# Optimization experiments

Hardware: AMD Instinct MI355X
Metric: run time of the kernel (lower is better)

## Reference

```python
import jax, jax.numpy as jnp
import numpy as np

K = 2048          # codes per class
NC = 8            # num_classes
CD = 256          # conv_dims
SP = 4            # latent spatial (28 -> 14 -> 7 -> 4)
D = CD * SP * SP  # 4096 codebook vector dim
N = 512           # RoIs


def _conv(x, W, b, stride, pad):
    y = jax.lax.conv_general_dilated(x, W, (stride, stride), [(pad, pad), (pad, pad)],
                                     dimension_numbers=('NCHW', 'OIHW', 'NCHW'))
    return y + b[None, :, None, None]


def _upsample2_ac(x):
    # bilinear upsample x2 with align_corners=True (torch nn.Upsample semantics)
    n, ch, H, W = x.shape
    Ho, Wo = 2 * H, 2 * W
    ys = jnp.arange(Ho) * (H - 1) / (Ho - 1)
    xs = jnp.arange(Wo) * (W - 1) / (Wo - 1)
    y0 = jnp.floor(ys).astype(jnp.int32); y1 = jnp.minimum(y0 + 1, H - 1)
    x0 = jnp.floor(xs).astype(jnp.int32); x1 = jnp.minimum(x0 + 1, W - 1)
    wy = (ys - y0).astype(x.dtype); wx = (xs - x0).astype(x.dtype)
    r = x[:, :, y0, :] * (1 - wy)[None, None, :, None] + x[:, :, y1, :] * wy[None, None, :, None]
    return r[:, :, :, x0] * (1 - wx)[None, None, None, :] + r[:, :, :, x1] * wx[None, None, None, :]


def setup_inputs() -> dict:
    key = jax.random.key(0)
    ks = jax.random.split(key, 20)
    s = 0.02
    inp = {
        'x': jax.random.normal(ks[0], (N, 1, 28, 28), jnp.float32),
        'We0': jax.random.normal(ks[1], (CD, 1, 3, 3), jnp.float32) * s,
        'be0': jnp.zeros((CD,), jnp.float32),
        'We1': jax.random.normal(ks[2], (CD, CD, 3, 3), jnp.float32) * s,
        'be1': jnp.zeros((CD,), jnp.float32),
        'We2': jax.random.normal(ks[3], (CD, CD, 3, 3), jnp.float32) * s,
        'be2': jnp.zeros((CD,), jnp.float32),
        'E': jax.random.normal(ks[4], (K * NC, D), jnp.float32) * s,
        'Wd0': jax.random.normal(ks[5], (CD, CD, 3, 3), jnp.float32) * s,
        'bd0': jnp.zeros((CD,), jnp.float32),
        'Wd1': jax.random.normal(ks[6], (CD, CD, 3, 3), jnp.float32) * s,
        'bd1': jnp.zeros((CD,), jnp.float32),
        'Wd2': jax.random.normal(ks[7], (CD, CD, 3, 3), jnp.float32) * s,
        'bd2': jnp.zeros((CD,), jnp.float32),
        'Wo': jax.random.normal(ks[8], (1, CD, 3, 3), jnp.float32) * s,
        'bo': jnp.zeros((1,), jnp.float32),
        'c': jax.random.randint(ks[9], (N,), 0, NC, jnp.int32),
    }
    return inp


def reference(x, We0, be0, We1, be1, We2, be2, E, Wd0, bd0, Wd1, bd1, Wd2, bd2, Wo, bo, c):
    # ---- encoder: 3 stride-2 convs, relu on all but the last ----
    h = jax.nn.relu(_conv(x, We0, be0, 2, 1))   # [N,CD,14,14]
    h = jax.nn.relu(_conv(h, We1, be1, 2, 1))   # [N,CD,7,7]
    h = _conv(h, We2, be2, 2, 1)                # [N,CD,4,4]
    z_e = h.reshape(N, D)                       # flattened latent, == z_e_x [N,D,1,1]

    # ---- class-conditional VQ ----
    # torch code loops over unique classes and concatenates -> output is in
    # stable-sorted-by-class order; replicate via stable argsort permutation.
    perm = jnp.argsort(c)  # stable
    # distances to the FULL table, then mask codes outside the sample's class slice
    d2 = (jnp.sum(z_e * z_e, axis=1, keepdims=True)         # [N,1]
          - 2.0 * z_e @ E.T                                  # [N,K*NC]
          + jnp.sum(E * E, axis=1)[None, :])
    code_cls = jnp.arange(K * NC, dtype=c.dtype) // K        # class of each code row
    d2 = jnp.where(code_cls[None, :] == c[:, None], d2, jnp.inf)
    idx = jnp.argmin(d2, axis=1)                             # global code index (includes key*K offset)

    q_det = jax.lax.stop_gradient(E)[idx]                    # vq_st uses detached codebook
    z_q_st = z_e + jax.lax.stop_gradient(q_det - z_e)        # straight-through
    z_q_bar = E[idx]                                         # gradient flows to codebook

    z_q_st_p = z_q_st[perm]
    z_q_bar_p = z_q_bar[perm]

    # ---- decoder: (upsample2 bilinear ac + conv + relu) x3, pad=0 on layer k==num_conv-2 ----
    xd = z_q_st_p.reshape(N, CD, SP, SP)
    xd = jax.nn.relu(_conv(_upsample2_ac(xd), Wd0, bd0, 1, 1))  # 4->8
    xd = jax.nn.relu(_conv(_upsample2_ac(xd), Wd1, bd1, 1, 0))  # 8->16->14
    xd = jax.nn.relu(_conv(_upsample2_ac(xd), Wd2, bd2, 1, 1))  # 14->28
    x_tilde = jax.nn.sigmoid(_conv(xd, Wo, bo, 1, 1))           # [N,1,28,28]

    return (x_tilde, z_e.reshape(N, D, 1, 1), z_q_bar_p.reshape(N, D, 1, 1))
```

## Files before the change

### kernel.cpp

```cpp
#include <hip/hip_runtime.h>
#include <hip/hip_bf16.h>
#include <cstdint>
#include <cstddef>

#define CDIV(a,b) (((a)+(b)-1)/(b))

typedef __attribute__((ext_vector_type(8))) short vbf8;
typedef __attribute__((ext_vector_type(4))) float vf4;

__device__ inline unsigned short f2bf(float f) {
  unsigned u = __float_as_uint(f);
  unsigned r = (u + 0x7fffu + ((u >> 16) & 1u)) >> 16;
  return (unsigned short)r;
}
__device__ inline float bf2f(unsigned short h) { return __uint_as_float(((unsigned)h) << 16); }

__global__ __launch_bounds__(256) void conv_e0_cl_kernel(
    const float* __restrict__ x, const float* __restrict__ W,
    const float* __restrict__ b, unsigned short* __restrict__ hi,
    unsigned short* __restrict__ lo)
{
  __shared__ float s_img[784];
  const int n = blockIdx.x;
  const int co = threadIdx.x;
  for (int i = threadIdx.x; i < 784; i += 256) s_img[i] = x[(size_t)n*784 + i];
  float w[9];
#pragma unroll
  for (int t = 0; t < 9; ++t) w[t] = W[co*9 + t];
  const float bb = b[co];
  __syncthreads();
  for (int p = 0; p < 196; ++p) {
    int y = p / 14, xo = p % 14;
    float a = bb;
#pragma unroll
    for (int t = 0; t < 9; ++t) {
      int yi = 2*y + t/3 - 1, xi = 2*xo + t%3 - 1;
      if (yi >= 0 && yi < 28 && xi >= 0 && xi < 28) a = fmaf(w[t], s_img[yi*28 + xi], a);
    }
    a = fmaxf(a, 0.f);
    unsigned short h = f2bf(a);
    size_t oidx = ((size_t)n*196 + p)*256 + co;
    hi[oidx] = h;
    lo[oidx] = f2bf(a - bf2f(h));
  }
}

__global__ __launch_bounds__(256) void wprep2_kernel(
    const float* __restrict__ W, unsigned short* __restrict__ Whi,
    unsigned short* __restrict__ Wlo)
{
  int idx = blockIdx.x*256 + threadIdx.x;
  if (idx >= 589824) return;
  int j   = idx & 7;
  int co  = (idx >> 3) & 255;
  int cig = (idx >> 11) & 31;
  int t   = idx >> 16;
  int ci  = cig*8 + j;
  float w = W[((size_t)co*256 + ci)*9 + t];
  unsigned short h = f2bf(w);
  Whi[idx] = h;
  Wlo[idx] = f2bf(w - bf2f(h));
}

template<int STRIDE, int HO, int WO, int X0, int WOP, int ROWS, int HI, int WI,
         int PAD, int ACT, int SPLIT, int OUTMODE>
__global__ __launch_bounds__(256, 2) void convmfma_kernel(
    const unsigned short* __restrict__ inT, const unsigned short* __restrict__ inTlo,
    const vbf8* __restrict__ Wt, const vbf8* __restrict__ Wtlo,
    const float* __restrict__ bias,
    unsigned short* __restrict__ outT, unsigned short* __restrict__ outTlo,
    float* __restrict__ outF)
{
  constexpr int NFM = ROWS*WOP/16;
  constexpr int RIN = (ROWS-1)*STRIDE + 3;
  constexpr int WS  = (WOP-1)*STRIDE + 3;
  constexpr int NG  = SPLIT ? 12 : 4;
  __shared__ vbf8 sA[RIN*WS*8];

  const int n  = blockIdx.x;
  const int y0 = blockIdx.y * ROWS;
  const int tid = threadIdx.x;
  const int lane = tid & 63;
  const int wv = tid >> 6;
  const int l15 = lane & 15;
  const int lq  = lane >> 4;
  const int cobase = wv * 64;

  int abase[NFM];
#pragma unroll
  for (int mf = 0; mf < NFM; ++mf) {
    int pos = mf*16 + l15;
    abase[mf] = (pos / WOP) * STRIDE * WS + (pos % WOP) * STRIDE;
  }

  vf4 acc[NFM][4];
#pragma unroll
  for (int mf = 0; mf < NFM; ++mf)
#pragma unroll
    for (int nf = 0; nf < 4; ++nf) acc[mf][nf] = (vf4){0.f, 0.f, 0.f, 0.f};

#pragma unroll 1
  for (int g = 0; g < NG; ++g) {
    const int cc = g & 3;
    const unsigned short* src = (SPLIT && g >= 8) ? inTlo : inT;
    const vbf8* wsrc = (SPLIT && g >= 4 && g < 8) ? Wtlo : Wt;
    for (int idx = tid; idx < RIN*WS*8; idx += 256) {
      int lin = idx >> 3, cig = idx & 7;
      int r = lin / WS, x = lin % WS;
      int yi = y0*STRIDE + r - PAD, xi = X0*STRIDE + x - PAD;
      vbf8 v = {0,0,0,0,0,0,0,0};
      if (yi >= 0 && yi < HI && xi >= 0 && xi < WI)
        v = *(const vbf8*)(src + ((((size_t)n*HI + yi)*WI + xi)*256 + cc*64 + cig*8));
      sA[(lin*8 + cig) ^ (lin & 7)] = v;
    }
    __syncthreads();
#pragma unroll
    for (int t = 0; t < 9; ++t) {
      const int dy = t/3, dx = t%3;
#pragma unroll
      for (int kk = 0; kk < 2; ++kk) {
        vbf8 bfr[4];
        const int cig_g = cc*8 + kk*4 + lq;
#pragma unroll
        for (int nf = 0; nf < 4; ++nf)
          bfr[nf] = wsrc[((size_t)t*32 + cig_g)*256 + cobase + nf*16 + l15];
        vbf8 af[NFM];
        const int cigl = kk*4 + lq;
#pragma unroll
        for (int mf = 0; mf < NFM; ++mf) {
          int lin = abase[mf] + dy*WS + dx;
          af[mf] = sA[(lin*8 + cigl) ^ (lin & 7)];
        }
#pragma unroll
        for (int mf = 0; mf < NFM; ++mf)
#pragma unroll
          for (int nf = 0; nf < 4; ++nf)
            acc[mf][nf] = __builtin_amdgcn_mfma_f32_16x16x32_bf16(af[mf], bfr[nf], acc[mf][nf], 0, 0, 0);
      }
    }
    __syncthreads();
  }

  float bb[4];
#pragma unroll
  for (int nf = 0; nf < 4; ++nf) bb[nf] = bias[cobase + nf*16 + l15];
#pragma unroll
  for (int mf = 0; mf < NFM; ++mf) {
#pragma unroll
    for (int q = 0; q < 4; ++q) {
      int pos = mf*16 + lq*4 + q;
      int y = y0 + pos/WOP, x = X0 + pos % WOP;
      if (X0 + WOP > WO && x >= WO) continue;
      if (HO % ROWS != 0 && y >= HO) continue;
#pragma unroll
      for (int nf = 0; nf < 4; ++nf) {
        float v = acc[mf][nf][q] + bb[nf];
        if (ACT) v = fmaxf(v, 0.f);
        const int co = cobase + nf*16 + l15;
        if (OUTMODE == 2) {
          outF[((size_t)n*256 + co)*(HO*WO) + y*WO + x] = v;
        } else {
          size_t oidx = (((size_t)n*HO + y)*WO + x)*256 + co;
          unsigned short h = f2bf(v);
          outT[oidx] = h;
          if (OUTMODE == 1) outTlo[oidx] = f2bf(v - bf2f(h));
        }
      }
    }
  }
}

template<int H, int W>
__global__ __launch_bounds__(256) void upsample_cl_kernel(
    const unsigned short* __restrict__ in, unsigned short* __restrict__ out, int nimg)
{
  constexpr int Ho = 2*H, Wo = 2*W;
  int idx = blockIdx.x*256 + threadIdx.x;
  int total = nimg * Ho * Wo * 32;
  if (idx >= total) return;
  int cig = idx & 31; int rest = idx >> 5;
  int xo = rest % Wo; rest /= Wo;
  int yo = rest % Ho; int n = rest / Ho;
  float ys = (float)(yo*(H-1)) / (float)(Ho-1);
  float xs = (float)(xo*(W-1)) / (float)(Wo-1);
  int ya = (int)ys; int yb = (ya+1 < H) ? ya+1 : H-1;
  int xa = (int)xs; int xb = (xa+1 < W) ? xa+1 : W-1;
  float wy = ys - (float)ya, wx = xs - (float)xa;
  const unsigned short* base = in + (size_t)n*H*W*256 + cig*8;
  vbf8 vaa = *(const vbf8*)(base + ((size_t)ya*W + xa)*256);
  vbf8 vab = *(const vbf8*)(base + ((size_t)ya*W + xb)*256);
  vbf8 vba = *(const vbf8*)(base + ((size_t)yb*W + xa)*256);
  vbf8 vbb = *(const vbf8*)(base + ((size_t)yb*W + xb)*256);
  vbf8 o;
#pragma unroll
  for (int j = 0; j < 8; ++j) {
    float r0 = bf2f((unsigned short)vaa[j])*(1.f-wy) + bf2f((unsigned short)vba[j])*wy;
    float r1 = bf2f((unsigned short)vab[j])*(1.f-wy) + bf2f((unsigned short)vbb[j])*wy;
    o[j] = (short)f2bf(r0*(1.f-wx) + r1*wx);
  }
  *(vbf8*)(out + (((size_t)n*Ho + yo)*Wo + xo)*256 + cig*8) = o;
}

__global__ __launch_bounds__(256) void conv_out_t_kernel(
    const unsigned short* __restrict__ a2t, const float* __restrict__ Wo,
    const float* __restrict__ bo, float* __restrict__ out)
{
  const int n = blockIdx.x;
  const int y0 = blockIdx.y * 14;
  const int tid = threadIdx.x;
  __shared__ vbf8 s_in[16*30*8];
  __shared__ float s_w[9*64];
  float acc[2] = {0.f, 0.f};
  for (int cc = 0; cc < 4; ++cc) {
    for (int idx = tid; idx < 16*30*8; idx += 256) {
      int lin = idx >> 3, cig = idx & 7;
      int r = lin / 30, xx = lin % 30;
      int yi = y0 + r - 1, xi = xx - 1;
      vbf8 v = {0,0,0,0,0,0,0,0};
      if (yi >= 0 && yi < 28 && xi >= 0 && xi < 28)
        v = *(const vbf8*)(a2t + (((size_t)n*28 + yi)*28 + xi)*256 + cc*64 + cig*8);
      s_in[(lin*8 + cig) ^ (lin & 7)] = v;
    }
    for (int idx = tid; idx < 576; idx += 256) {
      int t = idx / 64, cil = idx % 64;
      s_w[t*64 + cil] = Wo[((size_t)cc*64 + cil)*9 + t];
    }
    __syncthreads();
#pragma unroll
    for (int q = 0; q < 2; ++q) {
      int p = tid + q*256;
      if (p < 392) {
        int y = p / 28, x = p % 28;
        float a = acc[q];
#pragma unroll
        for (int t = 0; t < 9; ++t) {
          int lin = (y + t/3)*30 + (x + t%3);
#pragma unroll
          for (int cig = 0; cig < 8; ++cig) {
            vbf8 v = s_in[(lin*8 + cig) ^ (lin & 7)];
#pragma unroll
            for (int j = 0; j < 8; ++j)
              a = fmaf(bf2f((unsigned short)v[j]), s_w[t*64 + cig*8 + j], a);
          }
        }
        acc[q] = a;
      }
    }
    __syncthreads();
  }
  const float bb = bo[0];
  for (int q = 0; q < 2; ++q) {
    int p = tid + q*256;
    if (p < 392) {
      int y = y0 + p/28, x = p%28;
      out[(size_t)n*784 + y*28 + x] = 1.f/(1.f + expf(-(acc[q] + bb)));
    }
  }
}

__global__ __launch_bounds__(256) void enorm_kernel(
    const float* __restrict__ E, float* __restrict__ norms)
{
  const int k = blockIdx.x;
  const float4* row = (const float4*)(E + (size_t)k*4096);
  float s = 0.f;
  for (int i = threadIdx.x; i < 1024; i += 256) {
    float4 v = row[i];
    s += v.x*v.x + v.y*v.y + v.z*v.z + v.w*v.w;
  }
  __shared__ float red[256];
  red[threadIdx.x] = s; __syncthreads();
  for (int off = 128; off > 0; off >>= 1) {
    if (threadIdx.x < off) red[threadIdx.x] += red[threadIdx.x + off];
    __syncthreads();
  }
  if (threadIdx.x == 0) norms[k] = red[0];
}

__global__ __launch_bounds__(256) void etrans_kernel(
    const float* __restrict__ E, unsigned short* __restrict__ Et)
{
  const int cb = blockIdx.x;
  const int kb = blockIdx.y;
  const int t = threadIdx.x;
  const int cl = t >> 2;
  const int seg = t & 3;
  const int code = cb*64 + cl;
  const int k0 = kb*64 + seg*16;
  const float4* src = (const float4*)(E + (size_t)code*4096 + k0);
  float4 v0 = src[0], v1 = src[1], v2 = src[2], v3 = src[3];
  vbf8 a, b;
  a[0]=(short)f2bf(v0.x); a[1]=(short)f2bf(v0.y); a[2]=(short)f2bf(v0.z); a[3]=(short)f2bf(v0.w);
  a[4]=(short)f2bf(v1.x); a[5]=(short)f2bf(v1.y); a[6]=(short)f2bf(v1.z); a[7]=(short)f2bf(v1.w);
  b[0]=(short)f2bf(v2.x); b[1]=(short)f2bf(v2.y); b[2]=(short)f2bf(v2.z); b[3]=(short)f2bf(v2.w);
  b[4]=(short)f2bf(v3.x); b[5]=(short)f2bf(v3.y); b[6]=(short)f2bf(v3.z); b[7]=(short)f2bf(v3.w);
  vbf8* dst = (vbf8*)Et;
  dst[(size_t)(k0 >> 3)*16384 + code]     = a;
  dst[((size_t)(k0 >> 3) + 1)*16384 + code] = b;
}

__global__ __launch_bounds__(512) void perm_kernel(
    const int* __restrict__ c, int* __restrict__ perm, int* __restrict__ off)
{
  __shared__ int sc[512];
  __shared__ int cnt[8];
  __shared__ int base[9];
  const int i = threadIdx.x;
  sc[i] = c[i];
  if (i < 8) cnt[i] = 0;
  __syncthreads();
  atomicAdd(&cnt[sc[i]], 1);
  __syncthreads();
  if (i == 0) { int a = 0; for (int j = 0; j < 8; ++j) { base[j] = a; a += cnt[j]; } base[8] = a; }
  __syncthreads();
  const int ci = sc[i];
  int rank = 0;
  for (int j = 0; j < i; ++j) rank += (sc[j] == ci) ? 1 : 0;
  perm[base[ci] + rank] = i;
  if (i < 9) off[i] = base[i];
}

__global__ __launch_bounds__(256) void vq_coarse_kernel(
    const float* __restrict__ zE, const vbf8* __restrict__ Etv,
    const float* __restrict__ norms, const int* __restrict__ perm,
    const int* __restrict__ offs, float* __restrict__ dco)
{
  const int cls = blockIdx.x;
  const int mb  = blockIdx.y;
  const int kb  = blockIdx.z;
  const int s0 = offs[cls];
  const int total = offs[cls+1] - s0;
  int nrows = total - mb*64;
  if (nrows <= 0) return;
  if (nrows > 64) nrows = 64;

  __shared__ vbf8 sA[64*8];
  __shared__ int srow_s[64];
  const int tid = threadIdx.x;
  if (tid < 64) srow_s[tid] = (tid < nrows) ? perm[s0 + mb*64 + tid] : -1;
  __syncthreads();

  const int lane = tid & 63;
  const int wv = tid >> 6;
  const int l15 = lane & 15;
  const int lq  = lane >> 4;

  const int myrow = tid >> 2;
  const int seg = tid & 3;
  const int srow_mine = srow_s[myrow];
  const float* zbase = (srow_mine >= 0) ? (zE + (size_t)srow_mine*4096 + seg*16) : nullptr;

  const int cbase = cls*2048 + kb*256 + wv*64;

  vf4 acc[4][4];
#pragma unroll
  for (int mf = 0; mf < 4; ++mf)
#pragma unroll
    for (int nf = 0; nf < 4; ++nf) acc[mf][nf] = (vf4){0.f, 0.f, 0.f, 0.f};

#pragma unroll 1
  for (int k0 = 0; k0 < 4096; k0 += 64) {
    {
      float4 v0, v1, v2, v3;
      if (zbase) {
        const float4* p = (const float4*)(zbase + k0);
        v0 = p[0]; v1 = p[1]; v2 = p[2]; v3 = p[3];
      } else {
        v0 = v1 = v2 = v3 = (float4){0.f, 0.f, 0.f, 0.f};
      }
      vbf8 a, b;
      a[0]=(short)f2bf(v0.x); a[1]=(short)f2bf(v0.y); a[2]=(short)f2bf(v0.z); a[3]=(short)f2bf(v0.w);
      a[4]=(short)f2bf(v1.x); a[5]=(short)f2bf(v1.y); a[6]=(short)f2bf(v1.z); a[7]=(short)f2bf(v1.w);
      b[0]=(short)f2bf(v2.x); b[1]=(short)f2bf(v2.y); b[2]=(short)f2bf(v2.z); b[3]=(short)f2bf(v2.w);
      b[4]=(short)f2bf(v3.x); b[5]=(short)f2bf(v3.y); b[6]=(short)f2bf(v3.z); b[7]=(short)f2bf(v3.w);
      int c0 = seg*2;
      sA[myrow*8 + (c0 ^ (myrow & 7))]       = a;
      sA[myrow*8 + ((c0 + 1) ^ (myrow & 7))] = b;
    }
    __syncthreads();
#pragma unroll
    for (int kb32 = 0; kb32 < 2; ++kb32) {
      vbf8 af[4], bf[4];
#pragma unroll
      for (int mf = 0; mf < 4; ++mf) {
        int row = mf*16 + l15;
        af[mf] = sA[row*8 + ((kb32*4 + lq) ^ (row & 7))];
      }
      const size_t kg = (size_t)((k0 >> 3) + kb32*4 + lq);
#pragma unroll
      for (int nf = 0; nf < 4; ++nf)
        bf[nf] = Etv[kg*16384 + cbase + nf*16 + l15];
#pragma unroll
      for (int mf = 0; mf < 4; ++mf)
#pragma unroll
        for (int nf = 0; nf < 4; ++nf)
          acc[mf][nf] = __builtin_amdgcn_mfma_f32_16x16x32_bf16(af[mf], bf[nf], acc[mf][nf], 0, 0, 0);
    }
    __syncthreads();
  }

  float nrm[4];
#pragma unroll
  for (int nf = 0; nf < 4; ++nf) nrm[nf] = norms[cbase + nf*16 + l15];
#pragma unroll
  for (int mf = 0; mf < 4; ++mf) {
#pragma unroll
    for (int q = 0; q < 4; ++q) {
      int slot = mf*16 + lq*4 + q;
      if (slot < nrows) {
        int s = srow_s[slot];
        float* drow = dco + (size_t)s*2048 + (kb*256 + wv*64);
#pragma unroll
        for (int nf = 0; nf < 4; ++nf)
          drow[nf*16 + l15] = nrm[nf] - 2.f*acc[mf][nf][q];
      }
    }
  }
}

__global__ __launch_bounds__(256) void vq_select_kernel(
    const float* __restrict__ dco, const int* __restrict__ c,
    const float* __restrict__ zE, const float* __restrict__ E,
    int* __restrict__ codes)
{
  const int s = blockIdx.x;
  const int cls = c[s];
  const int tid = threadIdx.x;
  const float* drow = dco + (size_t)s*2048;

  float mn = 3.4e38f, mx = -3.4e38f;
  for (int j = tid; j < 2048; j += 256) {
    float d = drow[j];
    mn = fminf(mn, d); mx = fmaxf(mx, d);
  }
  __shared__ float smn[256], smx[256];
  smn[tid] = mn; smx[tid] = mx;
  __syncthreads();
  for (int o = 128; o > 0; o >>= 1) {
    if (tid < o) { smn[tid] = fminf(smn[tid], smn[tid+o]); smx[tid] = fmaxf(smx[tid], smx[tid+o]); }
    __syncthreads();
  }
  const float dmin = smn[0], dmax = smx[0];
  const float margin = 0.06f*(dmax - dmin) + 1e-6f*fabsf(dmin) + 1e-20f;

  __shared__ int cand[64];
  __shared__ int cnt_s;
  if (tid == 0) cnt_s = 0;
  __syncthreads();
  for (int j = tid; j < 2048; j += 256) {
    if (drow[j] <= dmin + margin) {
      int p = atomicAdd(&cnt_s, 1);
      if (p < 64) cand[p] = j;
    }
  }
  __syncthreads();
  const int cnt = (cnt_s < 64) ? cnt_s : 64;

  __shared__ double red[256];
  __shared__ double bestd_s;
  __shared__ int bestc_s;
  if (tid == 0) { bestd_s = 1.0e300; bestc_s = 0x7fffffff; }
  __syncthreads();
  const float* zrow = zE + (size_t)s*4096;
  for (int t = 0; t < cnt; ++t) {
    const int gcode = cls*2048 + cand[t];
    const float* erow = E + (size_t)gcode*4096;
    double p = 0.0;
    for (int e2 = tid; e2 < 4096; e2 += 256) {
      double ev = (double)erow[e2];
      double zv = (double)zrow[e2];
      p += ev*ev - 2.0*zv*ev;
    }
    red[tid] = p;
    __syncthreads();
    for (int o = 128; o > 0; o >>= 1) {
      if (tid < o) red[tid] += red[tid+o];
      __syncthreads();
    }
    if (tid == 0) {
      double d = red[0];
      if (d < bestd_s || (d == bestd_s && gcode < bestc_s)) { bestd_s = d; bestc_s = gcode; }
    }
    __syncthreads();
  }
  if (tid == 0) codes[s] = bestc_s;
}

__global__ __launch_bounds__(256) void gather_t_kernel(
    const int* __restrict__ codes, const int* __restrict__ perm,
    const float* __restrict__ E, float* __restrict__ zq, unsigned short* __restrict__ zqt)
{
  const int i = blockIdx.x;
  const int s = perm[i];
  const int code = codes[s];
  const float4* src = (const float4*)(E + (size_t)code*4096);
  float4* dst = (float4*)(zq + (size_t)i*4096);
  for (int t = threadIdx.x; t < 1024; t += 256) {
    float4 v = src[t];
    dst[t] = v;
    int e0 = t*4;
    int ci = e0 >> 4, sp = e0 & 15;
    unsigned short* zp = zqt + ((size_t)i*16 + sp)*256 + ci;
    zp[0]   = f2bf(v.x);
    zp[256] = f2bf(v.y);
    zp[512] = f2bf(v.z);
    zp[768] = f2bf(v.w);
  }
}

extern "C" void kernel_launch(void* const* d_in, const int* in_sizes, int n_in,
                              void* d_out, int out_size, void* d_ws, size_t ws_size,
                              hipStream_t stream) {
  const float* x   = (const float*)d_in[0];
  const float* We0 = (const float*)d_in[1];
  const float* be0 = (const float*)d_in[2];
  const float* We1 = (const float*)d_in[3];
  const float* be1 = (const float*)d_in[4];
  const float* We2 = (const float*)d_in[5];
  const float* be2 = (const float*)d_in[6];
  const float* E   = (const float*)d_in[7];
  const float* Wd0 = (const float*)d_in[8];
  const float* bd0 = (const float*)d_in[9];
  const float* Wd1 = (const float*)d_in[10];
  const float* bd1 = (const float*)d_in[11];
  const float* Wd2 = (const float*)d_in[12];
  const float* bd2 = (const float*)d_in[13];
  const float* Wo  = (const float*)d_in[14];
  const float* bo  = (const float*)d_in[15];
  const int*   c   = (const int*)d_in[16];

  float* out = (float*)d_out;
  float* z_e = out + (size_t)512*784;
  float* zq  = z_e + (size_t)512*4096;

  char* ws = (char*)d_ws;
  size_t off = 0;
  float* norms = (float*)(ws + off); off += 65536;
  int* codes = (int*)(ws + off); off += 2048;
  int* perm = (int*)(ws + off); off += 2048;
  int* offs = (int*)(ws + off); off += 256;
  float* dco = (float*)(ws + off); off += (size_t)512*2048*4;
  unsigned short* zqt = (unsigned short*)(ws + off); off += (size_t)512*16*256*2;
  unsigned short* Et = (unsigned short*)(ws + off); off += (size_t)512*16384*8*2;
  unsigned short* Wt0  = (unsigned short*)(ws + off); off += 1179648;
  unsigned short* Wt0l = (unsigned short*)(ws + off); off += 1179648;
  unsigned short* Wt1  = (unsigned short*)(ws + off); off += 1179648;
  unsigned short* Wt1l = (unsigned short*)(ws + off); off += 1179648;
  unsigned short* Wt2  = (unsigned short*)(ws + off); off += 1179648;
  unsigned short* Wt2l = (unsigned short*)(ws + off); off += 1179648;
  unsigned short* We1h = (unsigned short*)(ws + off); off += 1179648;
  unsigned short* We1l = (unsigned short*)(ws + off); off += 1179648;
  unsigned short* We2h = (unsigned short*)(ws + off); off += 1179648;
  unsigned short* We2l = (unsigned short*)(ws + off); off += 1179648;
  char* big = ws + off;
  size_t avail = (ws_size > off) ? ws_size - off : 0;

  int NB = 512;
  while (NB > 1 && (size_t)NB * 1350656ull > avail) NB >>= 1;
  const int nch = 512 / NB;

  size_t o = 0;
  unsigned short* h0h = (unsigned short*)(big + o); o += (size_t)NB*100352;
  unsigned short* h0l = (unsigned short*)(big + o); o += (size_t)NB*100352;
  unsigned short* h1h = (unsigned short*)(big + o); o += (size_t)NB*25088;
  unsigned short* h1l = (unsigned short*)(big + o); o += (size_t)NB*25088;
  unsigned short* u0t = (unsigned short*)(big + o); o += (size_t)NB*32768;
  unsigned short* a0t = (unsigned short*)(big + o); o += (size_t)NB*32768;
  unsigned short* u1t = (unsigned short*)(big + o); o += (size_t)NB*131072;
  unsigned short* a1t = (unsigned short*)(big + o); o += (size_t)NB*100352;
  unsigned short* u2t = (unsigned short*)(big + o); o += (size_t)NB*401408;
  unsigned short* a2t = (unsigned short*)(big + o); o += (size_t)NB*401408;

  wprep2_kernel<<<CDIV(589824,256), 256, 0, stream>>>(Wd0, Wt0, Wt0l);
  wprep2_kernel<<<CDIV(589824,256), 256, 0, stream>>>(Wd1, Wt1, Wt1l);
  wprep2_kernel<<<CDIV(589824,256), 256, 0, stream>>>(Wd2, Wt2, Wt2l);
  wprep2_kernel<<<CDIV(589824,256), 256, 0, stream>>>(We1, We1h, We1l);
  wprep2_kernel<<<CDIV(589824,256), 256, 0, stream>>>(We2, We2h, We2l);
  enorm_kernel<<<16384, 256, 0, stream>>>(E, norms);
  etrans_kernel<<<dim3(256,64), 256, 0, stream>>>(E, Et);

  for (int ch = 0; ch < nch; ++ch) {
    conv_e0_cl_kernel<<<NB, 256, 0, stream>>>(x + (size_t)ch*NB*784, We0, be0, h0h, h0l);
    convmfma_kernel<2,7,7,0,8,2, 14,14,1,1,1,1><<<dim3(NB,4), 256, 0, stream>>>(
        h0h, h0l, (const vbf8*)We1h, (const vbf8*)We1l, be1, h1h, h1l, nullptr);
    convmfma_kernel<2,4,4,0,4,4, 7,7,1,0,1,2><<<dim3(NB,1), 256, 0, stream>>>(
        h1h, h1l, (const vbf8*)We2h, (const vbf8*)We2l, be2, nullptr, nullptr,
        z_e + (size_t)ch*NB*4096);
  }
  perm_kernel<<<1, 512, 0, stream>>>(c, perm, offs);
  vq_coarse_kernel<<<dim3(8,8,8), 256, 0, stream>>>(
      z_e, (const vbf8*)Et, norms, perm, offs, dco);
  vq_select_kernel<<<512, 256, 0, stream>>>(dco, c, z_e, E, codes);
  gather_t_kernel<<<512, 256, 0, stream>>>(codes, perm, E, zq, zqt);

  for (int ch = 0; ch < nch; ++ch) {
    const unsigned short* zt = zqt + (size_t)ch*NB*16*256;
    upsample_cl_kernel<4,4><<<CDIV(NB*2048,256), 256, 0, stream>>>(zt, u0t, NB);
    convmfma_kernel<1,8,8,0,8,8, 8,8,1,1,0,0><<<dim3(NB,1), 256, 0, stream>>>(
        u0t, nullptr, (const vbf8*)Wt0, nullptr, bd0, a0t, nullptr, nullptr);
    upsample_cl_kernel<8,8><<<CDIV(NB*8192,256), 256, 0, stream>>>(a0t, u1t, NB);
    convmfma_kernel<1,14,14,0,16,4, 16,16,0,1,0,0><<<dim3(NB,4), 256, 0, stream>>>(
        u1t, nullptr, (const vbf8*)Wt1, nullptr, bd1, a1t, nullptr, nullptr);
    upsample_cl_kernel<14,14><<<CDIV(NB*25088,256), 256, 0, stream>>>(a1t, u2t, NB);
    convmfma_kernel<1,28,28,0,16,4, 28,28,1,1,0,0><<<dim3(NB,7), 256, 0, stream>>>(
        u2t, nullptr, (const vbf8*)Wt2, nullptr, bd2, a2t, nullptr, nullptr);
    convmfma_kernel<1,28,28,16,12,4, 28,28,1,1,0,0><<<dim3(NB,7), 256, 0, stream>>>(
        u2t, nullptr, (const vbf8*)Wt2, nullptr, bd2, a2t, nullptr, nullptr);
    conv_out_t_kernel<<<dim3(NB,2), 256, 0, stream>>>(a2t, Wo, bo, out + (size_t)ch*NB*784);
  }
}
```

Baseline: 1.969 ms.

## Double-buffer conv input tiles in LDS and retile encoder/decoder conv launches

```diff
diff --git a/kernel.cpp b/kernel.cpp
--- a/kernel.cpp
+++ b/kernel.cpp
@@ -62,8 +62,39 @@
   Wlo[idx] = f2bf(w - bf2f(h));
 }
 
+template<int NFM, int WS>
+__device__ __forceinline__ void mfma_block(
+    const vbf8* __restrict__ sbuf, const vbf8* __restrict__ wsrc, int cc,
+    const int (&abase)[NFM], vf4 (&acc)[NFM][4], int cobase, int l15, int lq)
+{
+#pragma unroll
+  for (int t = 0; t < 9; ++t) {
+    const int dy = t/3, dx = t%3;
+#pragma unroll
+    for (int kk = 0; kk < 2; ++kk) {
+      vbf8 bfr[4];
+      const int cig_g = cc*8 + kk*4 + lq;
+#pragma unroll
+      for (int nf = 0; nf < 4; ++nf)
+        bfr[nf] = wsrc[((size_t)t*32 + cig_g)*256 + cobase + nf*16 + l15];
+      vbf8 af[NFM];
+      const int cigl = kk*4 + lq;
+#pragma unroll
+      for (int mf = 0; mf < NFM; ++mf) {
+        int lin = abase[mf] + dy*WS + dx;
+        af[mf] = sbuf[(lin*8 + cigl) ^ (lin & 7)];
+      }
+#pragma unroll
+      for (int mf = 0; mf < NFM; ++mf)
+#pragma unroll
+        for (int nf = 0; nf < 4; ++nf)
+          acc[mf][nf] = __builtin_amdgcn_mfma_f32_16x16x32_bf16(af[mf], bfr[nf], acc[mf][nf], 0, 0, 0);
+    }
+  }
+}
+
 template<int STRIDE, int HO, int WO, int X0, int WOP, int ROWS, int HI, int WI,
-         int PAD, int ACT, int SPLIT, int OUTMODE>
+         int PAD, int ACT, int SPLIT, int OUTMODE, int DBUF>
 __global__ __launch_bounds__(256, 2) void convmfma_kernel(
     const unsigned short* __restrict__ inT, const unsigned short* __restrict__ inTlo,
     const vbf8* __restrict__ Wt, const vbf8* __restrict__ Wtlo,
@@ -75,7 +106,9 @@
   constexpr int RIN = (ROWS-1)*STRIDE + 3;
   constexpr int WS  = (WOP-1)*STRIDE + 3;
   constexpr int NG  = SPLIT ? 12 : 4;
-  __shared__ vbf8 sA[RIN*WS*8];
+  constexpr int NELEM = RIN*WS*8;
+  constexpr int CEIL = (NELEM + 255) / 256;
+  __shared__ vbf8 sA[DBUF ? 2 : 1][NELEM];
 
   const int n  = blockIdx.x;
   const int y0 = blockIdx.y * ROWS;
@@ -99,46 +132,73 @@
 #pragma unroll
     for (int nf = 0; nf < 4; ++nf) acc[mf][nf] = (vf4){0.f, 0.f, 0.f, 0.f};
 
+  if constexpr (DBUF) {
+    int goff[CEIL];
+#pragma unroll
+    for (int q = 0; q < CEIL; ++q) {
+      int idx = tid + q*256;
+      int lin = idx >> 3, cig = idx & 7;
+      int rr = lin / WS, xx = lin % WS;
+      int yi = y0*STRIDE + rr - PAD, xi = X0*STRIDE + xx - PAD;
+      bool ok = (idx < NELEM) && yi >= 0 && yi < HI && xi >= 0 && xi < WI;
+      goff[q] = ok ? (int)((((size_t)n*HI + yi)*WI + xi)*256 + cig*8) : -1;
+    }
+    vbf8 r[CEIL];
+#pragma unroll
+    for (int q = 0; q < CEIL; ++q) {
+      vbf8 v = {0,0,0,0,0,0,0,0};
+      if (goff[q] >= 0) v = *(const vbf8*)(inT + goff[q]);
+      r[q] = v;
+    }
+#pragma unroll
+    for (int q = 0; q < CEIL; ++q) {
+      int idx = tid + q*256;
+      if (idx < NELEM) { int lin = idx >> 3, cig = idx & 7; sA[0][(lin*8 + cig) ^ (lin & 7)] = r[q]; }
+    }
+    __syncthreads();
 #pragma unroll 1
-  for (int g = 0; g < NG; ++g) {
-    const int cc = g & 3;
-    const unsigned short* src = (SPLIT && g >= 8) ? inTlo : inT;
-    const vbf8* wsrc = (SPLIT && g >= 4 && g < 8) ? Wtlo : Wt;
-    for (int idx = tid; idx < RIN*WS*8; idx += 256) {
-      int lin = idx >> 3, cig = idx & 7;
-      int r = lin / WS, x = lin % WS;
-      int yi = y0*STRIDE + r - PAD, xi = X0*STRIDE + x - PAD;
-      vbf8 v = {0,0,0,0,0,0,0,0};
-      if (yi >= 0 && yi < HI && xi >= 0 && xi < WI)
-        v = *(const vbf8*)(src + ((((size_t)n*HI + yi)*WI + xi)*256 + cc*64 + cig*8));
-      sA[(lin*8 + cig) ^ (lin & 7)] = v;
-    }
-    __syncthreads();
-#pragma unroll
-    for (int t = 0; t < 9; ++t) {
-      const int dy = t/3, dx = t%3;
-#pragma unroll
-      for (int kk = 0; kk < 2; ++kk) {
-        vbf8 bfr[4];
-        const int cig_g = cc*8 + kk*4 + lq;
-#pragma unroll
-        for (int nf = 0; nf < 4; ++nf)
-          bfr[nf] = wsrc[((size_t)t*32 + cig_g)*256 + cobase + nf*16 + l15];
-        vbf8 af[NFM];
-        const int cigl = kk*4 + lq;
-#pragma unroll
-        for (int mf = 0; mf < NFM; ++mf) {
-          int lin = abase[mf] + dy*WS + dx;
-          af[mf] = sA[(lin*8 + cigl) ^ (lin & 7)];
+    for (int g = 0; g < NG; ++g) {
+      if (g + 1 < NG) {
+        const unsigned short* srcn = (SPLIT && (g+1) >= 8) ? inTlo : inT;
+        const int ccn64 = ((g+1) & 3) * 64;
+#pragma unroll
+        for (int q = 0; q < CEIL; ++q) {
+          vbf8 v = {0,0,0,0,0,0,0,0};
+          if (goff[q] >= 0) v = *(const vbf8*)(srcn + goff[q] + ccn64);
+          r[q] = v;
         }
-#pragma unroll
-        for (int mf = 0; mf < NFM; ++mf)
-#pragma unroll
-          for (int nf = 0; nf < 4; ++nf)
-            acc[mf][nf] = __builtin_amdgcn_mfma_f32_16x16x32_bf16(af[mf], bfr[nf], acc[mf][nf], 0, 0, 0);
-      }
-    }
-    __syncthreads();
+      }
+      const vbf8* wsrc = (SPLIT && g >= 4 && g < 8) ? Wtlo : Wt;
+      mfma_block<NFM, WS>(sA[g & 1], wsrc, g & 3, abase, acc, cobase, l15, lq);
+      if (g + 1 < NG) {
+        vbf8* nb = sA[(g+1) & 1];
+#pragma unroll
+        for (int q = 0; q < CEIL; ++q) {
+          int idx = tid + q*256;
+          if (idx < NELEM) { int lin = idx >> 3, cig = idx & 7; nb[(lin*8 + cig) ^ (lin & 7)] = r[q]; }
+        }
+      }
+      __syncthreads();
+    }
+  } else {
+#pragma unroll 1
+    for (int g = 0; g < NG; ++g) {
+      const int cc = g & 3;
+      const unsigned short* src = (SPLIT && g >= 8) ? inTlo : inT;
+      const vbf8* wsrc = (SPLIT && g >= 4 && g < 8) ? Wtlo : Wt;
+      for (int idx = tid; idx < NELEM; idx += 256) {
+        int lin = idx >> 3, cig = idx & 7;
+        int rr = lin / WS, xx = lin % WS;
+        int yi = y0*STRIDE + rr - PAD, xi = X0*STRIDE + xx - PAD;
+        vbf8 v = {0,0,0,0,0,0,0,0};
+        if (yi >= 0 && yi < HI && xi >= 0 && xi < WI)
+          v = *(const vbf8*)(src + ((((size_t)n*HI + yi)*WI + xi)*256 + cc*64 + cig*8));
+        sA[0][(lin*8 + cig) ^ (lin & 7)] = v;
+      }
+      __syncthreads();
+      mfma_block<NFM, WS>(sA[0], wsrc, cc, abase, acc, cobase, l15, lq);
+      __syncthreads();
+    }
   }
 
   float bb[4];
@@ -581,9 +641,9 @@
 
   for (int ch = 0; ch < nch; ++ch) {
     conv_e0_cl_kernel<<<NB, 256, 0, stream>>>(x + (size_t)ch*NB*784, We0, be0, h0h, h0l);
-    convmfma_kernel<2,7,7,0,8,2, 14,14,1,1,1,1><<<dim3(NB,4), 256, 0, stream>>>(
+    convmfma_kernel<2,7,7,0,8,4, 14,14,1,1,1,1, 1><<<dim3(NB,2), 256, 0, stream>>>(
         h0h, h0l, (const vbf8*)We1h, (const vbf8*)We1l, be1, h1h, h1l, nullptr);
-    convmfma_kernel<2,4,4,0,4,4, 7,7,1,0,1,2><<<dim3(NB,1), 256, 0, stream>>>(
+    convmfma_kernel<2,4,4,0,4,4, 7,7,1,0,1,2, 1><<<dim3(NB,1), 256, 0, stream>>>(
         h1h, h1l, (const vbf8*)We2h, (const vbf8*)We2l, be2, nullptr, nullptr,
         z_e + (size_t)ch*NB*4096);
   }
@@ -596,15 +656,13 @@
   for (int ch = 0; ch < nch; ++ch) {
     const unsigned short* zt = zqt + (size_t)ch*NB*16*256;
     upsample_cl_kernel<4,4><<<CDIV(NB*2048,256), 256, 0, stream>>>(zt, u0t, NB);
-    convmfma_kernel<1,8,8,0,8,8, 8,8,1,1,0,0><<<dim3(NB,1), 256, 0, stream>>>(
+    convmfma_kernel<1,8,8,0,8,8, 8,8,1,1,0,0, 1><<<dim3(NB,1), 256, 0, stream>>>(
         u0t, nullptr, (const vbf8*)Wt0, nullptr, bd0, a0t, nullptr, nullptr);
     upsample_cl_kernel<8,8><<<CDIV(NB*8192,256), 256, 0, stream>>>(a0t, u1t, NB);
-    convmfma_kernel<1,14,14,0,16,4, 16,16,0,1,0,0><<<dim3(NB,4), 256, 0, stream>>>(
+    convmfma_kernel<1,14,14,0,16,4, 16,16,0,1,0,0, 1><<<dim3(NB,4), 256, 0, stream>>>(
         u1t, nullptr, (const vbf8*)Wt1, nullptr, bd1, a1t, nullptr, nullptr);
     upsample_cl_kernel<14,14><<<CDIV(NB*25088,256), 256, 0, stream>>>(a1t, u2t, NB);
-    convmfma_kernel<1,28,28,0,16,4, 28,28,1,1,0,0><<<dim3(NB,7), 256, 0, stream>>>(
-        u2t, nullptr, (const vbf8*)Wt2, nullptr, bd2, a2t, nullptr, nullptr);
-    convmfma_kernel<1,28,28,16,12,4, 28,28,1,1,0,0><<<dim3(NB,7), 256, 0, stream>>>(
+    convmfma_kernel<1,28,28,0,28,4, 28,28,1,1,0,0, 0><<<dim3(NB,7), 256, 0, stream>>>(
         u2t, nullptr, (const vbf8*)Wt2, nullptr, bd2, a2t, nullptr, nullptr);
     conv_out_t_kernel<<<dim3(NB,2), 256, 0, stream>>>(a2t, Wo, bo, out + (size_t)ch*NB*784);
   }
```

Result: faster. 1.812 ms (-8.0%).
